# Kernel tuning notes

Hardware: AMD Instinct MI355X
Metric: run time of the kernel (lower is better)

## Reference

```python
import jax, jax.numpy as jnp
import numpy as np

N_NODES = 100000
N_EDGES = 600000
H_FEATS = 128


def setup_inputs() -> dict:
    key = jax.random.key(0)
    k_h, k_src, k_dst, k_w1, k_w2 = jax.random.split(key, 5)
    h = jax.random.normal(k_h, (N_NODES, H_FEATS), dtype=jnp.float32)
    src = jax.random.randint(k_src, (N_EDGES,), 0, N_NODES, dtype=jnp.int64)
    dst = jax.random.randint(k_dst, (N_EDGES,), 0, N_NODES, dtype=jnp.int64)
    # torch.nn.Linear-style params: out = x @ W.T + b
    W1_w = jax.random.normal(k_w1, (H_FEATS, 2 * H_FEATS), dtype=jnp.float32) * (1.0 / np.sqrt(2 * H_FEATS))
    W1_b = jnp.zeros((H_FEATS,), dtype=jnp.float32)
    W2_w = jax.random.normal(k_w2, (1, H_FEATS), dtype=jnp.float32) * (1.0 / np.sqrt(H_FEATS))
    W2_b = jnp.zeros((1,), dtype=jnp.float32)
    return {"h": h, "src": src, "dst": dst, "W1_w": W1_w, "W1_b": W1_b, "W2_w": W2_w, "W2_b": W2_b}


def reference(h, src, dst, W1_w, W1_b, W2_w, W2_b):
    # Gather endpoint features per edge and concatenate: [E, 2*h_feats]
    edge_feat = jnp.concatenate([h[src], h[dst]], axis=-1)
    # 2-layer MLP per edge: Linear -> ReLU -> Linear, scalar score per edge
    hid = jax.nn.relu(edge_feat @ W1_w.T + W1_b)  # [E, h_feats]
    score = hid @ W2_w.T + W2_b                   # [E, 1]
    return score[:, 0]                            # [E]
```

## Files before the change

kernel.cpp:

```cpp
#include <hip/hip_runtime.h>
#include <hip/hip_bf16.h>
#include <stdint.h>

typedef short bf16x8 __attribute__((ext_vector_type(8)));
typedef float f32x4  __attribute__((ext_vector_type(4)));

__device__ __forceinline__ ushort f2b(float f) {
  __hip_bfloat16 t = __float2bfloat16(f);
  return *reinterpret_cast<ushort*>(&t);
}
__device__ __forceinline__ bf16x8 pack8(float4 a, float4 b) {
  bf16x8 r;
  r[0]=(short)f2b(a.x); r[1]=(short)f2b(a.y); r[2]=(short)f2b(a.z); r[3]=(short)f2b(a.w);
  r[4]=(short)f2b(b.x); r[5]=(short)f2b(b.y); r[6]=(short)f2b(b.z); r[7]=(short)f2b(b.w);
  return r;
}

__global__ void repack_W1(const float* __restrict__ W1, int4* __restrict__ blob) {
  const int tid = blockIdx.x * 256 + threadIdx.x;
  const int l15  = tid & 15;
  const int lg   = (tid >> 4) & 3;
  const int kk   = (tid >> 6) & 3;
  const int nt   = (tid >> 8) & 7;
  const int half = (tid >> 11) & 1;
  const float* wp = W1 + (size_t)(nt * 16 + l15) * 256 + half * 128 + kk * 32 + lg * 8;
  const float4 fa = *(const float4*)wp;
  const float4 fb = *(const float4*)(wp + 4);
  bf16x8 r = pack8(fa, fb);
  blob[tid] = *reinterpret_cast<int4*>(&r);
}

__global__ __launch_bounds__(256, 2) void node_uv(
    const float* __restrict__ h, const int4* __restrict__ blob,
    const float* __restrict__ b1,
    uint8_t* __restrict__ u8, uint8_t* __restrict__ v8,
    float* __restrict__ su, float* __restrict__ sv,
    int Nn, int NT, int npairs, int niter)
{
  __shared__ ushort As[2][2048];

  const int t0   = threadIdx.x;
  const int w    = t0 >> 6;
  const int l    = t0 & 63;
  const int l15  = l & 15;
  const int lg   = l >> 4;
  const int pair = w >> 1;
  const int half = w & 1;
  const int gp   = blockIdx.x * 2 + pair;

  bf16x8 bfrag[8][4];
#pragma unroll
  for (int nt = 0; nt < 8; ++nt)
#pragma unroll
    for (int kk = 0; kk < 4; ++kk) {
      int4 x = blob[((half * 8 + nt) * 4 + kk) * 64 + l];
      bfrag[nt][kk] = *reinterpret_cast<bf16x8*>(&x);
    }

  float b1r[8];
#pragma unroll
  for (int nt = 0; nt < 8; ++nt) b1r[nt] = half ? 0.f : b1[nt * 16 + l15];

  uint8_t* __restrict__ outp = half ? v8 : u8;
  float*   __restrict__ outs = half ? sv : su;

  ushort* Ap = As[pair];
  const int pl = half * 64 + l;
  const float4* h4 = (const float4*)h;

  int t = gp;
  if (t < NT) {
    const size_t hb = (size_t)t * 512;
#pragma unroll
    for (int k = 0; k < 4; ++k) {
      const int i = k * 128 + pl, row = i >> 5, cc = i & 31;
      const int gr = t * 16 + row;
      float4 g = h4[gr < Nn ? hb + i : 0];
      ushort4 o; o.x = f2b(g.x); o.y = f2b(g.y); o.z = f2b(g.z); o.w = f2b(g.w);
      *(ushort4*)(Ap + row * 128 + (((cc >> 1) ^ (row & 7)) << 3) + (cc & 1) * 4) = o;
    }
  }
  __syncthreads();

  for (int it = 0; it < niter; ++it) {
    const int tn = t + npairs;

    float4 g[4];
    if (tn < NT) {
      const size_t hb = (size_t)tn * 512;
#pragma unroll
      for (int k = 0; k < 4; ++k) {
        const int i = k * 128 + pl;
        const int gr = tn * 16 + (i >> 5);
        g[k] = h4[gr < Nn ? hb + i : 0];
      }
    }

    if (t < NT) {
      f32x4 acc[8];
#pragma unroll
      for (int nt = 0; nt < 8; ++nt) acc[nt] = (f32x4){0.f, 0.f, 0.f, 0.f};

#pragma unroll
      for (int kk = 0; kk < 4; ++kk) {
        const int slot = (kk * 4 + lg) ^ (l15 & 7);
        int4 av = *(const int4*)(Ap + l15 * 128 + slot * 8);
        const bf16x8 a = *reinterpret_cast<bf16x8*>(&av);
#pragma unroll
        for (int nt = 0; nt < 8; ++nt)
          acc[nt] = __builtin_amdgcn_mfma_f32_16x16x32_bf16(a, bfrag[nt][kk], acc[nt], 0, 0, 0);
      }

      const int n0 = t * 16;
#pragma unroll
      for (int r = 0; r < 4; ++r) {
        float vals[8];
        float m = 1e-30f;
#pragma unroll
        for (int nt = 0; nt < 8; ++nt) {
          const float x = acc[nt][r] + b1r[nt];
          vals[nt] = x;
          m = fmaxf(m, fabsf(x));
        }
        m = fmaxf(m, __shfl_xor(m, 1));
        m = fmaxf(m, __shfl_xor(m, 2));
        m = fmaxf(m, __shfl_xor(m, 4));
        m = fmaxf(m, __shfl_xor(m, 8));
        const float inv = 127.0f * __builtin_amdgcn_rcpf(m);
        uint32_t lo = 0, hi = 0;
#pragma unroll
        for (int j = 0; j < 4; ++j) {
          const int q = (int)rintf(vals[j] * inv) + 128;
          lo |= (uint32_t)q << (8 * j);
        }
#pragma unroll
        for (int j = 0; j < 4; ++j) {
          const int q = (int)rintf(vals[4 + j] * inv) + 128;
          hi |= (uint32_t)q << (8 * j);
        }
        const int node = n0 + lg * 4 + r;
        if (node < Nn) {
          *(uint2*)(outp + (size_t)node * 128 + l15 * 8) = make_uint2(lo, hi);
          if (l15 == 0) outs[node] = m * (1.0f / 127.0f);
        }
      }
    }

    __syncthreads();
    if (tn < NT) {
#pragma unroll
      for (int k = 0; k < 4; ++k) {
        const int i = k * 128 + pl, row = i >> 5, cc = i & 31;
        ushort4 o; o.x = f2b(g[k].x); o.y = f2b(g[k].y); o.z = f2b(g[k].z); o.w = f2b(g[k].w);
        *(ushort4*)(Ap + row * 128 + (((cc >> 1) ^ (row & 7)) << 3) + (cc & 1) * 4) = o;
      }
    }
    __syncthreads();
    t = tn;
  }
}

__global__ __launch_bounds__(256) void edge_score_i8(
    const uint8_t* __restrict__ u8, const uint8_t* __restrict__ v8,
    const float* __restrict__ su, const float* __restrict__ sv,
    const int* __restrict__ src, const int* __restrict__ dst,
    const float* __restrict__ w2, const float* __restrict__ b2p,
    float* __restrict__ out, int E)
{
  const int t  = threadIdx.x;
  const int l  = t & 63;
  const int q  = l & 15;
  const int lg = l >> 4;

  float w2r[8];
#pragma unroll
  for (int j = 0; j < 8; ++j) w2r[j] = w2[j * 16 + q];
  const float b2 = b2p[0];

  const int gw = blockIdx.x * 4 + (t >> 6);
  const int TW = gridDim.x * 4;

  for (int base = gw * 16; base < E; base += TW * 16) {
    int e[4]; bool ok[4];
    uint2 ug[4], vg[4];
    float ss[4], sd[4];
#pragma unroll
    for (int i = 0; i < 4; ++i) {
      e[i]  = base + i * 4 + lg;
      ok[i] = e[i] < E;
      const int eS = ok[i] ? e[i] : 0;
      const int s = src[eS];
      const int d = dst[eS];
      ug[i] = *(const uint2*)(u8 + (size_t)s * 128 + q * 8);
      vg[i] = *(const uint2*)(v8 + (size_t)d * 128 + q * 8);
      ss[i] = su[s];
      sd[i] = sv[d];
    }
#pragma unroll
    for (int i = 0; i < 4; ++i) {
      const uint32_t ux = ug[i].x, uy = ug[i].y;
      const uint32_t vx = vg[i].x, vy = vg[i].y;
      const float bse = -128.0f * (ss[i] + sd[i]);
      float acc = 0.f;
#pragma unroll
      for (int j = 0; j < 4; ++j) {
        const float cu = (float)((ux >> (8 * j)) & 0xffu);
        const float cv = (float)((vx >> (8 * j)) & 0xffu);
        float x = fmaf(cu, ss[i], fmaf(cv, sd[i], bse));
        x = fmaxf(x, 0.f);
        acc = fmaf(x, w2r[j], acc);
      }
#pragma unroll
      for (int j = 0; j < 4; ++j) {
        const float cu = (float)((uy >> (8 * j)) & 0xffu);
        const float cv = (float)((vy >> (8 * j)) & 0xffu);
        float x = fmaf(cu, ss[i], fmaf(cv, sd[i], bse));
        x = fmaxf(x, 0.f);
        acc = fmaf(x, w2r[4 + j], acc);
      }
      acc += __shfl_xor(acc, 1);
      acc += __shfl_xor(acc, 2);
      acc += __shfl_xor(acc, 4);
      acc += __shfl_xor(acc, 8);
      if (q == 0 && ok[i]) out[e[i]] = acc + b2;
    }
  }
}

extern "C" void kernel_launch(void* const* d_in, const int* in_sizes, int n_in,
                              void* d_out, int out_size, void* d_ws, size_t ws_size,
                              hipStream_t stream) {
  const float* h   = (const float*)d_in[0];
  const int*   src = (const int*)d_in[1];
  const int*   dst = (const int*)d_in[2];
  const float* W1  = (const float*)d_in[3];
  const float* b1  = (const float*)d_in[4];
  const float* w2  = (const float*)d_in[5];
  const float* b2  = (const float*)d_in[6];
  float* out = (float*)d_out;

  const int nh = in_sizes[0];
  const int Nn = nh / 128;
  const int E  = in_sizes[1];

  uint8_t* ws = (uint8_t*)d_ws;
  int4*  blob = (int4*)ws;
  size_t off  = 65536;
  float* su   = (float*)(ws + off);  off += (size_t)Nn * 4;
  off = (off + 511) & ~(size_t)511;
  float* sv   = (float*)(ws + off);  off += (size_t)Nn * 4;
  off = (off + 511) & ~(size_t)511;
  uint8_t* u8 = ws + off;            off += (size_t)Nn * 128;
  uint8_t* v8 = ws + off;

  hipLaunchKernelGGL(repack_W1, dim3(16), dim3(256), 0, stream, W1, blob);

  const int NT     = (Nn + 15) / 16;
  const int nblk1  = 768;
  const int npairs = nblk1 * 2;
  const int niter  = (NT + npairs - 1) / npairs;
  hipLaunchKernelGGL(node_uv, dim3(nblk1), dim3(256), 0, stream,
                     h, blob, b1, u8, v8, su, sv, Nn, NT, npairs, niter);

  hipLaunchKernelGGL(edge_score_i8, dim3(2048), dim3(256), 0, stream,
                     u8, v8, su, sv, src, dst, w2, b2, out, E);
}
```

Baseline: 61.33 us.

## Split node GEMM output columns across wave pairs, raising occupancy with per-half scales

Each block now handles one 16-node tile, and four waves split the work: two waves per half (u or v), each computing 64 output columns. This halves the B fragments held in registers, so the launch bound rises to 4 blocks per CU with 1024 blocks. Each column half gets its own int8 quantisation scale, so su/sv double in size and the edge kernel loads them as float2. The goal is lower register pressure and more latency hiding in the node pass, paid for with extra scale traffic in the edge pass.

```diff
diff --git a/kernel.cpp b/kernel.cpp
--- a/kernel.cpp
+++ b/kernel.cpp
@@ -30,96 +30,94 @@
   blob[tid] = *reinterpret_cast<int4*>(&r);
 }
 
-__global__ __launch_bounds__(256, 2) void node_uv(
+__global__ __launch_bounds__(256, 4) void node_uv(
     const float* __restrict__ h, const int4* __restrict__ blob,
     const float* __restrict__ b1,
     uint8_t* __restrict__ u8, uint8_t* __restrict__ v8,
     float* __restrict__ su, float* __restrict__ sv,
-    int Nn, int NT, int npairs, int niter)
+    int Nn, int NT, int nblocks, int niter)
 {
-  __shared__ ushort As[2][2048];
+  __shared__ ushort As[2048];
 
   const int t0   = threadIdx.x;
   const int w    = t0 >> 6;
   const int l    = t0 & 63;
   const int l15  = l & 15;
   const int lg   = l >> 4;
-  const int pair = w >> 1;
-  const int half = w & 1;
-  const int gp   = blockIdx.x * 2 + pair;
-
-  bf16x8 bfrag[8][4];
-#pragma unroll
-  for (int nt = 0; nt < 8; ++nt)
+  const int half = w >> 1;
+  const int hw   = w & 1;
+
+  bf16x8 bfrag[4][4];
+#pragma unroll
+  for (int ntl = 0; ntl < 4; ++ntl)
 #pragma unroll
     for (int kk = 0; kk < 4; ++kk) {
-      int4 x = blob[((half * 8 + nt) * 4 + kk) * 64 + l];
-      bfrag[nt][kk] = *reinterpret_cast<bf16x8*>(&x);
-    }
-
-  float b1r[8];
-#pragma unroll
-  for (int nt = 0; nt < 8; ++nt) b1r[nt] = half ? 0.f : b1[nt * 16 + l15];
+      int4 x = blob[((half * 8 + hw * 4 + ntl) * 4 + kk) * 64 + l];
+      bfrag[ntl][kk] = *reinterpret_cast<bf16x8*>(&x);
+    }
+
+  float b1r[4];
+#pragma unroll
+  for (int ntl = 0; ntl < 4; ++ntl)
+    b1r[ntl] = half ? 0.f : b1[hw * 64 + ntl * 16 + l15];
 
   uint8_t* __restrict__ outp = half ? v8 : u8;
   float*   __restrict__ outs = half ? sv : su;
 
-  ushort* Ap = As[pair];
-  const int pl = half * 64 + l;
   const float4* h4 = (const float4*)h;
 
-  int t = gp;
+  int t = blockIdx.x;
   if (t < NT) {
     const size_t hb = (size_t)t * 512;
 #pragma unroll
-    for (int k = 0; k < 4; ++k) {
-      const int i = k * 128 + pl, row = i >> 5, cc = i & 31;
+    for (int k = 0; k < 2; ++k) {
+      const int i = k * 256 + t0, row = i >> 5, c = i & 31;
       const int gr = t * 16 + row;
       float4 g = h4[gr < Nn ? hb + i : 0];
       ushort4 o; o.x = f2b(g.x); o.y = f2b(g.y); o.z = f2b(g.z); o.w = f2b(g.w);
-      *(ushort4*)(Ap + row * 128 + (((cc >> 1) ^ (row & 7)) << 3) + (cc & 1) * 4) = o;
+      *(ushort4*)(As + row * 128 + (((c >> 1) ^ (row & 7)) << 3) + (c & 1) * 4) = o;
     }
   }
   __syncthreads();
 
   for (int it = 0; it < niter; ++it) {
-    const int tn = t + npairs;
-
-    float4 g[4];
+    const int tn = t + nblocks;
+
+    float4 g[2];
     if (tn < NT) {
       const size_t hb = (size_t)tn * 512;
 #pragma unroll
-      for (int k = 0; k < 4; ++k) {
-        const int i = k * 128 + pl;
+      for (int k = 0; k < 2; ++k) {
+        const int i = k * 256 + t0;
         const int gr = tn * 16 + (i >> 5);
         g[k] = h4[gr < Nn ? hb + i : 0];
       }
     }
 
     if (t < NT) {
-      f32x4 acc[8];
-#pragma unroll
-      for (int nt = 0; nt < 8; ++nt) acc[nt] = (f32x4){0.f, 0.f, 0.f, 0.f};
+      f32x4 acc[4];
+#pragma unroll
+      for (int ntl = 0; ntl < 4; ++ntl) acc[ntl] = (f32x4){0.f, 0.f, 0.f, 0.f};
 
 #pragma unroll
       for (int kk = 0; kk < 4; ++kk) {
         const int slot = (kk * 4 + lg) ^ (l15 & 7);
-        int4 av = *(const int4*)(Ap + l15 * 128 + slot * 8);
+        int4 av = *(const int4*)(As + l15 * 128 + slot * 8);
         const bf16x8 a = *reinterpret_cast<bf16x8*>(&av);
 #pragma unroll
-        for (int nt = 0; nt < 8; ++nt)
-          acc[nt] = __builtin_amdgcn_mfma_f32_16x16x32_bf16(a, bfrag[nt][kk], acc[nt], 0, 0, 0);
+        for (int ntl = 0; ntl < 4; ++ntl)
+          acc[ntl] = __builtin_amdgcn_mfma_f32_16x16x32_bf16(a, bfrag[ntl][kk], acc[ntl], 0, 0, 0);
       }
 
       const int n0 = t * 16;
 #pragma unroll
       for (int r = 0; r < 4; ++r) {
-        float vals[8];
+        float vals[4];
         float m = 1e-30f;
 #pragma unroll
-        for (int nt = 0; nt < 8; ++nt) {
-          const float x = acc[nt][r] + b1r[nt];
-          vals[nt] = x;
+        for (int ntl = 0; ntl < 4; ++ntl) {
+          const float x = acc[ntl][r] + b1r[ntl];
+          vals[ntl] = x;
           m = fmaxf(m, fabsf(x));
         }
         m = fmaxf(m, __shfl_xor(m, 1));
@@ -127,21 +125,16 @@
         m = fmaxf(m, __shfl_xor(m, 4));
         m = fmaxf(m, __shfl_xor(m, 8));
         const float inv = 127.0f * __builtin_amdgcn_rcpf(m);
-        uint32_t lo = 0, hi = 0;
+        uint32_t pk = 0;
 #pragma unroll
         for (int j = 0; j < 4; ++j) {
           const int q = (int)rintf(vals[j] * inv) + 128;
-          lo |= (uint32_t)q << (8 * j);
-        }
-#pragma unroll
-        for (int j = 0; j < 4; ++j) {
-          const int q = (int)rintf(vals[4 + j] * inv) + 128;
-          hi |= (uint32_t)q << (8 * j);
+          pk |= (uint32_t)q << (8 * j);
         }
         const int node = n0 + lg * 4 + r;
         if (node < Nn) {
-          *(uint2*)(outp + (size_t)node * 128 + l15 * 8) = make_uint2(lo, hi);
-          if (l15 == 0) outs[node] = m * (1.0f / 127.0f);
+          *(uint32_t*)(outp + (size_t)node * 128 + l15 * 8 + hw * 4) = pk;
+          if (l15 == 0) outs[node * 2 + hw] = m * (1.0f / 127.0f);
         }
       }
     }
@@ -149,10 +142,10 @@
     __syncthreads();
     if (tn < NT) {
 #pragma unroll
-      for (int k = 0; k < 4; ++k) {
-        const int i = k * 128 + pl, row = i >> 5, cc = i & 31;
+      for (int k = 0; k < 2; ++k) {
+        const int i = k * 256 + t0, row = i >> 5, c = i & 31;
         ushort4 o; o.x = f2b(g[k].x); o.y = f2b(g[k].y); o.z = f2b(g[k].z); o.w = f2b(g[k].w);
-        *(ushort4*)(Ap + row * 128 + (((cc >> 1) ^ (row & 7)) << 3) + (cc & 1) * 4) = o;
+        *(ushort4*)(As + row * 128 + (((c >> 1) ^ (row & 7)) << 3) + (c & 1) * 4) = o;
       }
     }
     __syncthreads();
@@ -179,11 +172,13 @@
 
   const int gw = blockIdx.x * 4 + (t >> 6);
   const int TW = gridDim.x * 4;
+  const float2* su2 = (const float2*)su;
+  const float2* sv2 = (const float2*)sv;
 
   for (int base = gw * 16; base < E; base += TW * 16) {
     int e[4]; bool ok[4];
     uint2 ug[4], vg[4];
-    float ss[4], sd[4];
+    float2 ss[4], sd[4];
 #pragma unroll
     for (int i = 0; i < 4; ++i) {
       e[i]  = base + i * 4 + lg;
@@ -193,20 +188,21 @@
       const int d = dst[eS];
       ug[i] = *(const uint2*)(u8 + (size_t)s * 128 + q * 8);
       vg[i] = *(const uint2*)(v8 + (size_t)d * 128 + q * 8);
-      ss[i] = su[s];
-      sd[i] = sv[d];
+      ss[i] = su2[s];
+      sd[i] = sv2[d];
     }
 #pragma unroll
     for (int i = 0; i < 4; ++i) {
       const uint32_t ux = ug[i].x, uy = ug[i].y;
       const uint32_t vx = vg[i].x, vy = vg[i].y;
-      const float bse = -128.0f * (ss[i] + sd[i]);
+      const float bse0 = -128.0f * (ss[i].x + sd[i].x);
+      const float bse1 = -128.0f * (ss[i].y + sd[i].y);
       float acc = 0.f;
 #pragma unroll
       for (int j = 0; j < 4; ++j) {
         const float cu = (float)((ux >> (8 * j)) & 0xffu);
         const float cv = (float)((vx >> (8 * j)) & 0xffu);
-        float x = fmaf(cu, ss[i], fmaf(cv, sd[i], bse));
+        float x = fmaf(cu, ss[i].x, fmaf(cv, sd[i].x, bse0));
         x = fmaxf(x, 0.f);
         acc = fmaf(x, w2r[j], acc);
       }
@@ -214,7 +210,7 @@
       for (int j = 0; j < 4; ++j) {
         const float cu = (float)((uy >> (8 * j)) & 0xffu);
         const float cv = (float)((vy >> (8 * j)) & 0xffu);
-        float x = fmaf(cu, ss[i], fmaf(cv, sd[i], bse));
+        float x = fmaf(cu, ss[i].y, fmaf(cv, sd[i].y, bse1));
         x = fmaxf(x, 0.f);
         acc = fmaf(x, w2r[4 + j], acc);
       }
@@ -246,21 +242,20 @@
   uint8_t* ws = (uint8_t*)d_ws;
   int4*  blob = (int4*)ws;
   size_t off  = 65536;
-  float* su   = (float*)(ws + off);  off += (size_t)Nn * 4;
+  float* su   = (float*)(ws + off);  off += (size_t)Nn * 8;
   off = (off + 511) & ~(size_t)511;
-  float* sv   = (float*)(ws + off);  off += (size_t)Nn * 4;
+  float* sv   = (float*)(ws + off);  off += (size_t)Nn * 8;
   off = (off + 511) & ~(size_t)511;
   uint8_t* u8 = ws + off;            off += (size_t)Nn * 128;
   uint8_t* v8 = ws + off;
 
   hipLaunchKernelGGL(repack_W1, dim3(16), dim3(256), 0, stream, W1, blob);
 
-  const int NT     = (Nn + 15) / 16;
-  const int nblk1  = 768;
-  const int npairs = nblk1 * 2;
-  const int niter  = (NT + npairs - 1) / npairs;
-  hipLaunchKernelGGL(node_uv, dim3(nblk1), dim3(256), 0, stream,
-                     h, blob, b1, u8, v8, su, sv, Nn, NT, npairs, niter);
+  const int NT      = (Nn + 15) / 16;
+  const int nblocks = 1024;
+  const int niter   = (NT + nblocks - 1) / nblocks;
+  hipLaunchKernelGGL(node_uv, dim3(nblocks), dim3(256), 0, stream,
+                     h, blob, b1, u8, v8, su, sv, Nn, NT, nblocks, niter);
 
   hipLaunchKernelGGL(edge_score_i8, dim3(2048), dim3(256), 0, stream,
                      u8, v8, su, sv, src, dst, w2, b2, out, E);
```

New measurement: 60.17 us. No clear change (-1.9%).
